# Performance work log

Hardware: AMD Instinct MI355X
Metric: run time of the kernel (lower is better)

Reference implementation:

```python
import jax, jax.numpy as jnp
import numpy as np

N_NODES = 50000
N_EDGES = 800000
IN_DIM = 128
ATT_DIM = 128
NEG_SLOPE = 0.01  # nn.LeakyReLU default


def setup_inputs() -> dict:
    key = jax.random.key(0)
    ks = jax.random.split(key, 8)
    x = jax.random.normal(ks[0], (N_NODES, IN_DIM), dtype=jnp.float32)
    src_idx = jax.random.randint(ks[1], (N_EDGES,), 0, N_NODES, dtype=jnp.int32)
    dst_idx = jax.random.randint(ks[2], (N_EDGES,), 0, N_NODES, dtype=jnp.int32)
    # small init scale keeps exp(score) numerically tame
    src_w = jax.random.normal(ks[3], (IN_DIM, ATT_DIM), dtype=jnp.float32) * 0.05
    src_b = jnp.zeros((ATT_DIM,), dtype=jnp.float32)
    dst_w = jax.random.normal(ks[4], (IN_DIM, ATT_DIM), dtype=jnp.float32) * 0.05
    dst_b = jnp.zeros((ATT_DIM,), dtype=jnp.float32)
    att_w = jax.random.normal(ks[5], (ATT_DIM, 1), dtype=jnp.float32) * 0.05
    att_b = jnp.zeros((1,), dtype=jnp.float32)
    return {"x": x, "src_idx": src_idx, "dst_idx": dst_idx,
            "src_w": src_w, "src_b": src_b, "dst_w": dst_w, "dst_b": dst_b,
            "att_w": att_w, "att_b": att_b}


def reference(x, src_idx, dst_idx, src_w, src_b, dst_w, dst_b, att_w, att_b):
    n = x.shape[0]
    # 1) mean aggregation of source features onto destinations (copy_u + mean)
    deg = jax.ops.segment_sum(jnp.ones_like(dst_idx, dtype=x.dtype), dst_idx, num_segments=n)
    h_mean = jax.ops.segment_sum(x[src_idx], dst_idx, num_segments=n)
    h_mean = h_mean / jnp.maximum(deg, 1.0)[:, None]
    # 2) attention projections on nodes (dense GEMMs)
    ha_src = x @ src_w + src_b          # [N, att_dim]
    ha_dst = h_mean @ dst_w + dst_b     # [N, att_dim]
    # 3) per-edge u_add_v -> LeakyReLU -> att Linear -> exp
    e = jax.nn.leaky_relu(ha_src[src_idx] + ha_dst[dst_idx], NEG_SLOPE)  # [E, att_dim]
    s = jnp.exp(e @ att_w + att_b)      # [E, 1]
    # 4) edge softmax: normalize by segment sum over destination
    denom = jax.ops.segment_sum(s, dst_idx, num_segments=n)  # [N, 1]
    a = s / denom[dst_idx]              # [E, 1]
    # 5) u_mul_e weighted aggregation (sum)
    out = jax.ops.segment_sum(x[src_idx] * a, dst_idx, num_segments=n)  # [N, in_dim]
    return out
```

## Files before the change

kernel.cpp:

```cpp
#include <hip/hip_runtime.h>
#include <math.h>

#define N_NODES 50000
#define N_EDGES 800000
#define DIM 128
#define NEG_SLOPE 0.01f
#define CAP 64
#define DEGS 32

#define GEMM_BLOCKS 3125
#define SCAT_BLOCKS 3125
#define MERGED_BLOCKS (GEMM_BLOCKS + SCAT_BLOCKS)

typedef short v8s __attribute__((ext_vector_type(8)));
typedef float v4f __attribute__((ext_vector_type(4)));
typedef float v2f __attribute__((ext_vector_type(2)));

__device__ inline unsigned f2bf2(float a, float b) {
    unsigned ua = __float_as_uint(a);
    unsigned ub = __float_as_uint(b);
    ua = (ua + 0x7fffu + ((ua >> 16) & 1u)) >> 16;
    ub = (ub + 0x7fffu + ((ub >> 16) & 1u)) & 0xffff0000u;
    return ua | ub;
}
__device__ inline v2f bf2v(unsigned u) {
    v2f r;
    r.x = __uint_as_float(u << 16);
    r.y = __uint_as_float(u & 0xffff0000u);
    return r;
}
__device__ inline v2f lk2(v2f v) {
    return __builtin_elementwise_max(v, v * NEG_SLOPE);
}

#define ROR_ADD(v, CTRL) \
    ((v) + __int_as_float(__builtin_amdgcn_update_dpp( \
        0, __float_as_int(v), (CTRL), 0xf, 0xf, false)))

__global__ __launch_bounds__(256) void k_prepw(
    const float* __restrict__ src_w, const float* __restrict__ dst_w,
    unsigned* __restrict__ whT, int* __restrict__ deg)
{
    int gid = blockIdx.x * 256 + threadIdx.x;
    if (gid < 256 * 64) {
        int n = gid >> 6;
        int kk = gid & 63;
        const float* W = (n < 128) ? src_w : dst_w;
        int col = n & 127;
        float w0 = W[(2 * kk) * DIM + col];
        float w1 = W[(2 * kk + 1) * DIM + col];
        whT[gid] = f2bf2(w0, w1);
    }
    if (gid < N_NODES) deg[gid * DEGS] = 0;
}

__global__ __launch_bounds__(64) void k_scatgemm(
    const int* __restrict__ src, const int* __restrict__ dst,
    int* __restrict__ deg, int* __restrict__ slots,
    const float* __restrict__ x, const unsigned* __restrict__ whT,
    const float* __restrict__ src_b, unsigned* __restrict__ hx_u,
    unsigned* __restrict__ yu)
{
    __shared__ unsigned L[16][132];
    int b = blockIdx.x;
    int lane = threadIdx.x;

    if (b & 1) {
        int bs = b >> 1;
        int e0 = bs * 256 + lane;
        int sv[4], dv[4], pos[4];
        #pragma unroll
        for (int i = 0; i < 4; ++i) {
            sv[i] = src[e0 + i * 64];
            dv[i] = dst[e0 + i * 64];
        }
        #pragma unroll
        for (int i = 0; i < 4; ++i)
            pos[i] = atomicAdd(&deg[dv[i] * DEGS], 1);
        #pragma unroll
        for (int i = 0; i < 4; ++i)
            if (pos[i] < CAP) slots[dv[i] * CAP + pos[i]] = sv[i] * 64;
        return;
    }

    int bx = b >> 1;
    int quad = lane >> 4;
    int m = lane & 15;

    int arow = bx * 16 + m;
    const float4* xp = (const float4*)(x + (size_t)arow * DIM + quad * 8);
    float4 f[4][2];
    #pragma unroll
    for (int k0 = 0; k0 < 4; ++k0) {
        f[k0][0] = xp[k0 * 8];
        f[k0][1] = xp[k0 * 8 + 1];
    }

    v8s bb[4];
    #pragma unroll
    for (int k0 = 0; k0 < 4; ++k0) {
        union { unsigned u[4]; v8s s; } pk;
        pk.u[0] = f2bf2(f[k0][0].x, f[k0][0].y);
        pk.u[1] = f2bf2(f[k0][0].z, f[k0][0].w);
        pk.u[2] = f2bf2(f[k0][1].x, f[k0][1].y);
        pk.u[3] = f2bf2(f[k0][1].z, f[k0][1].w);
        bb[k0] = pk.s;
        int c = k0 * 32 + quad * 8 + 1;
        L[m][c + 0] = pk.u[0];
        L[m][c + 2] = pk.u[1];
        L[m][c + 4] = pk.u[2];
        L[m][c + 6] = pk.u[3];
    }

    v4f yacc[8];
    #pragma unroll
    for (int nt = 0; nt < 16; ++nt) {
        v4f acc = {0.f, 0.f, 0.f, 0.f};
        const uint4* ap = (const uint4*)(whT + (size_t)(nt * 16 + m) * 64 + quad * 4);
        #pragma unroll
        for (int k0 = 0; k0 < 4; ++k0) {
            union { uint4 u; v8s s; } af;
            af.u = ap[k0 * 4];
            acc = __builtin_amdgcn_mfma_f32_16x16x32_bf16(af.s, bb[k0], acc, 0, 0, 0);
        }
        if (nt < 8) {
            float4 bia = ((const float4*)src_b)[nt * 4 + quad];
            int c = nt * 16 + quad * 4;
            L[m][c]     = f2bf2(acc[0] + bia.x, acc[1] + bia.y);
            L[m][c + 2] = f2bf2(acc[2] + bia.z, acc[3] + bia.w);
        } else {
            yacc[nt - 8] = acc;
        }
    }

    int rbase0 = bx * 16;
    for (int i = lane; i < 512; i += 64) {
        int r = i >> 5, c = i & 31;
        ((uint4*)(hx_u + (size_t)(rbase0 + r) * 128))[c] = *(const uint4*)&L[r][c * 4];
    }

    #pragma unroll
    for (int t = 0; t < 8; ++t) {
        int c = t * 8 + quad * 2;
        L[m][c]     = f2bf2(yacc[t][0], yacc[t][1]);
        L[m][c + 1] = f2bf2(yacc[t][2], yacc[t][3]);
    }
    for (int i = lane; i < 256; i += 64) {
        int r = i >> 4, c = i & 15;
        ((uint4*)(yu + (size_t)(rbase0 + r) * 64))[c] = *(const uint4*)&L[r][c * 4];
    }
}

__global__ __launch_bounds__(256) void k_fuse(
    const uint2* __restrict__ hx, const unsigned* __restrict__ yu,
    const int* __restrict__ slots, const int* __restrict__ deg,
    const float* __restrict__ dst_b, const float* __restrict__ att_w,
    const float* __restrict__ att_b, float* __restrict__ out)
{
    int g = blockIdx.x * 256 + threadIdx.x;
    int node = g >> 6;
    int lane = g & 63;
    int grp = lane >> 4;
    int sl = lane & 15;
    int cnt = deg[node * DEGS];
    if (cnt == 0) {
        if (grp < 2) {
            v4f z = {0.f, 0.f, 0.f, 0.f};
            __builtin_nontemporal_store(z, (v4f*)out + node * 32 + (grp ? 16 + sl : sl));
        }
        return;
    }
    int cc = (cnt < CAP) ? cnt : CAP;
    int trips = (cc + 3) >> 2;
    int myoff = (lane < cc) ? slots[node * CAP + lane] : 0;

    v2f hd01 = {0.f, 0.f}, hd23 = {0.f, 0.f};
    v2f hd45 = {0.f, 0.f}, hd67 = {0.f, 0.f};
    #pragma unroll 4
    for (int t = 0; t < trips; ++t) {
        int i = 4 * t + grp;
        bool valid = (i < cc);
        int off = __shfl(myoff, valid ? i : 0);
        if (valid) {
            const uint2* yp = (const uint2*)(yu + off);
            uint2 qa = yp[sl];
            uint2 qb = yp[16 + sl];
            hd01 += bf2v(qa.x);
            hd23 += bf2v(qa.y);
            hd45 += bf2v(qb.x);
            hd67 += bf2v(qb.y);
        }
    }
    float inv = 1.0f / (float)cnt;
    float m0 = hd01.x, m1 = hd01.y, m2 = hd23.x, m3 = hd23.y;
    float m4 = hd45.x, m5 = hd45.y, m6 = hd67.x, m7 = hd67.y;
    #define XRED(f) { f += __shfl_xor(f, 32); f += __shfl_xor(f, 16); f *= inv; }
    XRED(m0) XRED(m1) XRED(m2) XRED(m3) XRED(m4) XRED(m5) XRED(m6) XRED(m7)
    #undef XRED
    float4 db0 = ((const float4*)dst_b)[sl];
    float4 db1 = ((const float4*)dst_b)[16 + sl];
    hd01 = (v2f){m0 + db0.x, m1 + db0.y};
    hd23 = (v2f){m2 + db0.z, m3 + db0.w};
    hd45 = (v2f){m4 + db1.x, m5 + db1.y};
    hd67 = (v2f){m6 + db1.z, m7 + db1.w};

    float4 aw0f = ((const float4*)att_w)[sl];
    float4 aw1f = ((const float4*)att_w)[16 + sl];
    v2f aw01 = (v2f){aw0f.x, aw0f.y}, aw23 = (v2f){aw0f.z, aw0f.w};
    v2f aw45 = (v2f){aw1f.x, aw1f.y}, aw67 = (v2f){aw1f.z, aw1f.w};
    float ab = att_b[0];
    v2f o01 = {0.f, 0.f}, o23 = {0.f, 0.f};
    v2f o45 = {0.f, 0.f}, o67 = {0.f, 0.f};
    float dsum = 0.f;
    #pragma unroll 4
    for (int t = 0; t < trips; ++t) {
        int i = 4 * t + grp;
        bool valid = (i < cc);
        int off = __shfl(myoff, valid ? i : 0);
        if (valid) {
            const uint4* hp = (const uint4*)(hx + off);
            uint4 qa = hp[sl];
            uint4 qb = hp[16 + sl];
            v2f p2 = {0.f, 0.f};
            p2 = __builtin_elementwise_fma(lk2(bf2v(qa.x) + hd01), aw01, p2);
            p2 = __builtin_elementwise_fma(lk2(bf2v(qa.z) + hd23), aw23, p2);
            p2 = __builtin_elementwise_fma(lk2(bf2v(qb.x) + hd45), aw45, p2);
            p2 = __builtin_elementwise_fma(lk2(bf2v(qb.z) + hd67), aw67, p2);
            float p = p2.x + p2.y;
            p = ROR_ADD(p, 0x128);
            p = ROR_ADD(p, 0x124);
            p = ROR_ADD(p, 0x122);
            p = ROR_ADD(p, 0x121);
            float s = __expf(p + ab);
            v2f s2 = (v2f){s, s};
            o01 = __builtin_elementwise_fma(bf2v(qa.y), s2, o01);
            o23 = __builtin_elementwise_fma(bf2v(qa.w), s2, o23);
            o45 = __builtin_elementwise_fma(bf2v(qb.y), s2, o45);
            o67 = __builtin_elementwise_fma(bf2v(qb.w), s2, o67);
            dsum += s;
        }
    }
    dsum += __shfl_xor(dsum, 32);
    dsum += __shfl_xor(dsum, 16);
    float r0 = o01.x, r1 = o01.y, r2 = o23.x, r3 = o23.y;
    float r4 = o45.x, r5 = o45.y, r6 = o67.x, r7 = o67.y;
    #define XRED2(f) { f += __shfl_xor(f, 32); f += __shfl_xor(f, 16); }
    XRED2(r0) XRED2(r1) XRED2(r2) XRED2(r3) XRED2(r4) XRED2(r5) XRED2(r6) XRED2(r7)
    #undef XRED2
    float r = 1.0f / dsum;
    if (grp < 2) {
        v4f ov;
        if (grp == 0) {
            ov[0] = r0 * r; ov[1] = r1 * r; ov[2] = r2 * r; ov[3] = r3 * r;
            __builtin_nontemporal_store(ov, (v4f*)out + node * 32 + sl);
        } else {
            ov[0] = r4 * r; ov[1] = r5 * r; ov[2] = r6 * r; ov[3] = r7 * r;
            __builtin_nontemporal_store(ov, (v4f*)out + node * 32 + 16 + sl);
        }
    }
}

extern "C" void kernel_launch(void* const* d_in, const int* in_sizes, int n_in,
                              void* d_out, int out_size, void* d_ws, size_t ws_size,
                              hipStream_t stream)
{
    const float* x     = (const float*)d_in[0];
    const int*   src   = (const int*)d_in[1];
    const int*   dst   = (const int*)d_in[2];
    const float* src_w = (const float*)d_in[3];
    const float* src_b = (const float*)d_in[4];
    const float* dst_w = (const float*)d_in[5];
    const float* dst_b = (const float*)d_in[6];
    const float* att_w = (const float*)d_in[7];
    const float* att_b = (const float*)d_in[8];
    float* out = (float*)d_out;
    (void)in_sizes; (void)n_in; (void)out_size; (void)ws_size;

    const size_t NF = (size_t)N_NODES * DIM;

    int* ws = (int*)d_ws;
    int* ideg  = ws;
    int* slots = ws + 1600512;
    unsigned* whT = (unsigned*)(ws + 4800512);
    unsigned* yu  = whT + 16384;
    uint2*    hx  = (uint2*)(yu + NF / 2);

    k_prepw<<<256, 256, 0, stream>>>(src_w, dst_w, whT, ideg);

    k_scatgemm<<<MERGED_BLOCKS, 64, 0, stream>>>(
        src, dst, ideg, slots, x, whT, src_b, (unsigned*)hx, yu);

    k_fuse<<<N_NODES * 64 / 256, 256, 0, stream>>>(
        hx, yu, slots, ideg, dst_b, att_w, att_b, out);
}
```

Baseline: 242.0 us.

## Pack three GEMM waves and one scatter wave into each 256-thread block

Replaces the alternating one-wave GEMM and scatter blocks with 256-thread blocks. Three waves each compute a 16-row GEMM tile and the fourth wave does the CSR scatter for 768 edges, with bounds checks added for the ragged tail. The aim is to cut block count and launch overhead and to co-schedule the atomic scatter with MFMA work inside one CU. The trade-off is that the scatter wave now serially handles 12 edges per lane, so it can become the longest-running wave in each block.

```diff
diff --git a/kernel.cpp b/kernel.cpp
--- a/kernel.cpp
+++ b/kernel.cpp
@@ -8,9 +8,9 @@
 #define CAP 64
 #define DEGS 32
 
-#define GEMM_BLOCKS 3125
-#define SCAT_BLOCKS 3125
-#define MERGED_BLOCKS (GEMM_BLOCKS + SCAT_BLOCKS)
+#define SG_BLOCKS 1042
+#define ROWS_PB 48
+#define EPB 768
 
 typedef short v8s __attribute__((ext_vector_type(8)));
 typedef float v4f __attribute__((ext_vector_type(4)));
@@ -54,46 +54,60 @@
     if (gid < N_NODES) deg[gid * DEGS] = 0;
 }
 
-__global__ __launch_bounds__(64) void k_scatgemm(
+__global__ __launch_bounds__(256) void k_scatgemm(
     const int* __restrict__ src, const int* __restrict__ dst,
     int* __restrict__ deg, int* __restrict__ slots,
     const float* __restrict__ x, const unsigned* __restrict__ whT,
     const float* __restrict__ src_b, unsigned* __restrict__ hx_u,
     unsigned* __restrict__ yu)
 {
-    __shared__ unsigned L[16][132];
+    __shared__ unsigned L3[3][16][132];
     int b = blockIdx.x;
-    int lane = threadIdx.x;
-
-    if (b & 1) {
-        int bs = b >> 1;
-        int e0 = bs * 256 + lane;
-        int sv[4], dv[4], pos[4];
-        #pragma unroll
-        for (int i = 0; i < 4; ++i) {
-            sv[i] = src[e0 + i * 64];
-            dv[i] = dst[e0 + i * 64];
-        }
-        #pragma unroll
-        for (int i = 0; i < 4; ++i)
-            pos[i] = atomicAdd(&deg[dv[i] * DEGS], 1);
-        #pragma unroll
-        for (int i = 0; i < 4; ++i)
+    int tid = threadIdx.x;
+    int wave = tid >> 6;
+    int lane = tid & 63;
+
+    if (wave == 3) {
+        int e0 = b * EPB + lane;
+        int sv[12], dv[12], pos[12];
+        #pragma unroll
+        for (int i = 0; i < 12; ++i) {
+            int e = e0 + i * 64;
+            bool v = (e < N_EDGES);
+            sv[i] = v ? src[e] : 0;
+            dv[i] = v ? dst[e] : 0;
+        }
+        #pragma unroll
+        for (int i = 0; i < 12; ++i) {
+            int e = e0 + i * 64;
+            pos[i] = (e < N_EDGES) ? atomicAdd(&deg[dv[i] * DEGS], 1) : CAP;
+        }
+        #pragma unroll
+        for (int i = 0; i < 12; ++i)
             if (pos[i] < CAP) slots[dv[i] * CAP + pos[i]] = sv[i] * 64;
         return;
     }
 
-    int bx = b >> 1;
+    unsigned (*L)[132] = L3[wave];
     int quad = lane >> 4;
     int m = lane & 15;
-
-    int arow = bx * 16 + m;
-    const float4* xp = (const float4*)(x + (size_t)arow * DIM + quad * 8);
+    int rbase0 = b * ROWS_PB + wave * 16;
+    int arow = rbase0 + m;
+    bool live = (arow < N_NODES);
+
     float4 f[4][2];
     #pragma unroll
     for (int k0 = 0; k0 < 4; ++k0) {
-        f[k0][0] = xp[k0 * 8];
-        f[k0][1] = xp[k0 * 8 + 1];
+        f[k0][0] = make_float4(0.f, 0.f, 0.f, 0.f);
+        f[k0][1] = f[k0][0];
+    }
+    if (live) {
+        const float4* xp = (const float4*)(x + (size_t)arow * DIM + quad * 8);
+        #pragma unroll
+        for (int k0 = 0; k0 < 4; ++k0) {
+            f[k0][0] = xp[k0 * 8];
+            f[k0][1] = xp[k0 * 8 + 1];
+        }
     }
 
     v8s bb[4];
@@ -133,10 +147,11 @@
         }
     }
 
-    int rbase0 = bx * 16;
     for (int i = lane; i < 512; i += 64) {
         int r = i >> 5, c = i & 31;
-        ((uint4*)(hx_u + (size_t)(rbase0 + r) * 128))[c] = *(const uint4*)&L[r][c * 4];
+        int row = rbase0 + r;
+        if (row < N_NODES)
+            ((uint4*)(hx_u + (size_t)row * 128))[c] = *(const uint4*)&L[r][c * 4];
     }
 
     #pragma unroll
@@ -147,7 +162,9 @@
     }
     for (int i = lane; i < 256; i += 64) {
         int r = i >> 4, c = i & 15;
-        ((uint4*)(yu + (size_t)(rbase0 + r) * 64))[c] = *(const uint4*)&L[r][c * 4];
+        int row = rbase0 + r;
+        if (row < N_NODES)
+            ((uint4*)(yu + (size_t)row * 64))[c] = *(const uint4*)&L[r][c * 4];
     }
 }
 
@@ -287,7 +304,7 @@
 
     k_prepw<<<256, 256, 0, stream>>>(src_w, dst_w, whT, ideg);
 
-    k_scatgemm<<<MERGED_BLOCKS, 64, 0, stream>>>(
+    k_scatgemm<<<SG_BLOCKS, 256, 0, stream>>>(
         src, dst, ideg, slots, x, whT, src_b, (unsigned*)hx, yu);
 
     k_fuse<<<N_NODES * 64 / 256, 256, 0, stream>>>(
```

New measurement: 236.1 us. -2.5%, faster.
